# Kernel tuning notes

Measured on AMD Instinct MI355X. Metric: run time of the kernel, lower is better.

## Reference

```python
import jax, jax.numpy as jnp
import numpy as np
from jax import lax

B, L, H, KSIZE = 8, 16384, 128, 65
PAD = KSIZE // 2  # 32; odd kernel keeps output length == L


def setup_inputs() -> dict:
    key = jax.random.key(0)
    kq, kk, kv, kw = jax.random.split(key, 4)
    Q = jax.random.normal(kq, (B, L, H), dtype=jnp.float32)
    K = jax.random.normal(kk, (B, L, H), dtype=jnp.float32)
    V = jax.random.normal(kv, (B, L, H), dtype=jnp.float32)
    # Conv1d weight [out_ch, in_ch, kernel], kaiming-like scale
    W = jax.random.normal(kw, (H, H, KSIZE), dtype=jnp.float32) / np.sqrt(H * KSIZE)
    return {"Q": Q, "K": K, "V": V, "W": W}


def reference(Q, K, V, W):
    # [B, L, H] -> [B, H, L] (channels-first, matching torch transpose(1,2))
    Qt = jnp.swapaxes(Q, 1, 2)
    Kt = jnp.swapaxes(K, 1, 2)
    Vt = jnp.swapaxes(V, 1, 2)
    # Conv1d over sequence dim; lax conv is cross-correlation like torch
    conv_q = lax.conv_general_dilated(
        Qt, W,
        window_strides=(1,),
        padding=[(PAD, PAD)],
        dimension_numbers=("NCH", "OIH", "NCH"),
    )  # [B, H, L]
    scores = conv_q * Kt                      # elementwise gate
    A = jax.nn.softmax(scores, axis=-1)       # softmax over sequence dim
    Z = A * Vt                                # weighted V (elementwise)
    return jnp.swapaxes(Z, 1, 2)              # back to [B, L, H]
```

## Files before the change

kernel.cpp:

```cpp
#include <hip/hip_runtime.h>
#include <stdint.h>

#define BATCH 8
#define LSEQ 16384
#define HDIM 128
#define KSZ 65
#define PADW 32
#define LH (LSEQ*HDIM)
#define TL 256
#define NROWS (TL + 2*PADW)
#define LBLKS (LSEQ/TL)
#define EXP_SHIFT 20.0f
#define SLOT 16384

#define WS_WBF_OFF 4096

typedef __attribute__((ext_vector_type(8))) short bf16x8;
typedef __attribute__((ext_vector_type(4))) short bf16x4;
typedef __attribute__((ext_vector_type(16))) float f32x16;

__device__ __forceinline__ unsigned short f2bf(float f) {
  unsigned int u = __float_as_uint(f);
  return (unsigned short)((u + 0x7FFFu + ((u >> 16) & 1u)) >> 16);
}

__global__ __launch_bounds__(256) void wcvt_kernel(const float* __restrict__ W,
                                                   unsigned short* __restrict__ Wbf) {
  __shared__ float lw[KSZ*HDIM];
  const int o = blockIdx.x;
  const float* src = W + (size_t)o * (HDIM*KSZ);
  for (int t = threadIdx.x; t < HDIM*KSZ; t += 256) lw[t] = src[t];
  __syncthreads();
  const int ob  = o >> 5;
  const int l31 = o & 31;
  for (int idx = threadIdx.x; idx < KSZ*HDIM; idx += 256) {
    const int k = idx >> 7;
    const int i = idx & 127;
    const int kk  = i >> 4;
    const int hi2 = (i >> 3) & 1;
    const int e   = i & 7;
    const size_t dst = (size_t)k*SLOT + kk*2048 + ob*512 + hi2*256 + l31*8 + e;
    Wbf[dst] = f2bf(lw[i*KSZ + k]);
  }
}

__device__ __forceinline__ void stage_tap(const unsigned short* __restrict__ gsrc,
                                          char* lbase, int w, int lane) {
  const char* gb = (const char*)gsrc;
#pragma unroll
  for (int r = 0; r < 4; ++r) {
    const int off = r*8192 + w*1024;
    __builtin_amdgcn_global_load_lds(
        (const __attribute__((address_space(1))) unsigned int*)(gb + off + lane*16),
        (__attribute__((address_space(3))) unsigned int*)(lbase + off),
        16, 0, 0);
  }
}

__global__ __launch_bounds__(512, 2) void conv_gate_kernel(
    const float* __restrict__ Qm, const float* __restrict__ Km,
    const unsigned short* __restrict__ Wfrag,
    float* __restrict__ Eout, float* __restrict__ gsum) {

  __shared__ __align__(16) char smem[147456];
  unsigned short* Qs = (unsigned short*)smem;
  char* WsBase = smem + 81920;

  const int tid  = threadIdx.x;
  const int lane = tid & 63;
  const int w    = tid >> 6;
  const int ks   = w & 1;
  const int wc   = (w >> 1) & 1;
  const int wr   = w >> 2;
  const int l31  = lane & 31;
  const int hi2  = lane >> 5;

  const int bx = blockIdx.x;
  const int b  = bx >> 6;
  const int l0 = (bx & 63) << 8;

  {
    const int r0 = tid >> 5;
    const int c4 = (tid & 31) << 2;
    const float* qbase = Qm + (size_t)b*LH + c4;
#pragma unroll
    for (int it = 0; it < NROWS/16; ++it) {
      const int r = it*16 + r0;
      const int grow = l0 - PADW + r;
      bf16x4 pk = {0, 0, 0, 0};
      if (grow >= 0 && grow < LSEQ) {
        const float4 qv = *(const float4*)(qbase + (size_t)grow*HDIM);
        pk[0] = (short)f2bf(qv.x); pk[1] = (short)f2bf(qv.y);
        pk[2] = (short)f2bf(qv.z); pk[3] = (short)f2bf(qv.w);
      }
      *(bf16x4*)(&Qs[r*HDIM + (c4 ^ ((r & 15) << 3))]) = pk;
    }
  }

  stage_tap(Wfrag, WsBase, w, lane);

  f32x16 acc[4][2] = {};

  __syncthreads();

  const int arow0 = wr*128 + l31;
  const int bbase = (wc*2)*512 + lane*8;

#define LOADC(c, A0,A1,A2,A3,B0,B1) { \
    const int i0 = (ks*64 + (c)*16 + hi2*8) ^ xa; \
    A0 = *(const bf16x8*)(&Qs[(rb     )*HDIM + i0]); \
    A1 = *(const bf16x8*)(&Qs[(rb + 32)*HDIM + i0]); \
    A2 = *(const bf16x8*)(&Qs[(rb + 64)*HDIM + i0]); \
    A3 = *(const bf16x8*)(&Qs[(rb + 96)*HDIM + i0]); \
    B0 = *(const bf16x8*)(&slot[(ks*4 + (c))*2048 + bbase]); \
    B1 = *(const bf16x8*)(&slot[(ks*4 + (c))*2048 + bbase + 512]); \
  }
#define MM(A0,A1,A2,A3,B0,B1) \
    acc[0][0] = __builtin_amdgcn_mfma_f32_32x32x16_bf16(A0, B0, acc[0][0], 0, 0, 0); \
    acc[0][1] = __builtin_amdgcn_mfma_f32_32x32x16_bf16(A0, B1, acc[0][1], 0, 0, 0); \
    acc[1][0] = __builtin_amdgcn_mfma_f32_32x32x16_bf16(A1, B0, acc[1][0], 0, 0, 0); \
    acc[1][1] = __builtin_amdgcn_mfma_f32_32x32x16_bf16(A1, B1, acc[1][1], 0, 0, 0); \
    acc[2][0] = __builtin_amdgcn_mfma_f32_32x32x16_bf16(A2, B0, acc[2][0], 0, 0, 0); \
    acc[2][1] = __builtin_amdgcn_mfma_f32_32x32x16_bf16(A2, B1, acc[2][1], 0, 0, 0); \
    acc[3][0] = __builtin_amdgcn_mfma_f32_32x32x16_bf16(A3, B0, acc[3][0], 0, 0, 0); \
    acc[3][1] = __builtin_amdgcn_mfma_f32_32x32x16_bf16(A3, B1, acc[3][1], 0, 0, 0);

  for (int k = 0; k < KSZ; ++k) {
    const unsigned short* slot = (const unsigned short*)(WsBase + (k & 1)*32768);
    if (k < KSZ-1)
      stage_tap(Wfrag + (size_t)(k+1)*SLOT, WsBase + ((k+1) & 1)*32768, w, lane);

    const int rb = k + arow0;
    const int xa = (rb & 15) << 3;

    bf16x8 a0,a1,a2,a3,b0,b1, c0,c1,c2,c3,d0,d1;
    LOADC(0, a0,a1,a2,a3,b0,b1)
    LOADC(1, c0,c1,c2,c3,d0,d1)
    MM(a0,a1,a2,a3,b0,b1)
    LOADC(2, a0,a1,a2,a3,b0,b1)
    MM(c0,c1,c2,c3,d0,d1)
    LOADC(3, c0,c1,c2,c3,d0,d1)
    MM(a0,a1,a2,a3,b0,b1)
    MM(c0,c1,c2,c3,d0,d1)

    asm volatile("s_waitcnt vmcnt(0)" ::: "memory");
    __builtin_amdgcn_s_barrier();
  }
#undef LOADC
#undef MM

  float* red = (float*)smem;
  const int widx = wr*2 + wc;
  float* reg = red + widx*8192 + lane*4;
  if (ks == 1) {
#pragma unroll
    for (int e4 = 0; e4 < 32; ++e4) {
      const int mfr = e4 >> 3, nf = (e4 >> 2) & 1, r4 = (e4 & 3) << 2;
      float4 v;
      v.x = acc[mfr][nf][r4];   v.y = acc[mfr][nf][r4+1];
      v.z = acc[mfr][nf][r4+2]; v.w = acc[mfr][nf][r4+3];
      *(float4*)(reg + e4*256) = v;
    }
  }
  __syncthreads();

  if (ks == 0) {
#pragma unroll
    for (int e4 = 0; e4 < 32; ++e4) {
      const int mfr = e4 >> 3, nf = (e4 >> 2) & 1, r4 = (e4 & 3) << 2;
      const float4 v = *(const float4*)(reg + e4*256);
      acc[mfr][nf][r4]   += v.x; acc[mfr][nf][r4+1] += v.y;
      acc[mfr][nf][r4+2] += v.z; acc[mfr][nf][r4+3] += v.w;
    }
    float psum[2] = {0.f, 0.f};
#pragma unroll
    for (int mfr = 0; mfr < 4; ++mfr) {
#pragma unroll
      for (int r = 0; r < 16; ++r) {
        const int row = wr*128 + mfr*32 + (r & 3) + 8*(r >> 2) + 4*hi2;
        const size_t gb = (size_t)b*LH + (size_t)(l0 + row)*HDIM + wc*64 + l31;
#pragma unroll
        for (int nf = 0; nf < 2; ++nf) {
          const float s = acc[mfr][nf][r] * Km[gb + nf*32];
          const float e = __expf(s - EXP_SHIFT);
          Eout[gb + nf*32] = e;
          psum[nf] += e;
        }
      }
    }
    psum[0] += __shfl_xor(psum[0], 32);
    psum[1] += __shfl_xor(psum[1], 32);
    if (hi2 == 0) {
      atomicAdd(&gsum[b*HDIM + wc*64 + l31],      psum[0]);
      atomicAdd(&gsum[b*HDIM + wc*64 + 32 + l31], psum[1]);
    }
  }
}

__global__ __launch_bounds__(256) void finalize_kernel(float* __restrict__ out,
                                                       const float* __restrict__ V,
                                                       const float* __restrict__ gsum) {
  const int total4 = (BATCH*LH) >> 2;
  const int stride = gridDim.x * blockDim.x;
  for (int f = blockIdx.x*blockDim.x + threadIdx.x; f < total4; f += stride) {
    const float4 e = ((const float4*)out)[f];
    const float4 v = ((const float4*)V)[f];
    const int e0 = f << 2;
    const float* gs = gsum + ((e0 >> 21) << 7) + (e0 & 127);
    float4 z;
    z.x = e.x * v.x / gs[0];
    z.y = e.y * v.y / gs[1];
    z.z = e.z * v.z / gs[2];
    z.w = e.w * v.w / gs[3];
    ((float4*)out)[f] = z;
  }
}

extern "C" void kernel_launch(void* const* d_in, const int* in_sizes, int n_in,
                              void* d_out, int out_size, void* d_ws, size_t ws_size,
                              hipStream_t stream) {
  (void)in_sizes; (void)n_in; (void)out_size; (void)ws_size;
  const float* Q = (const float*)d_in[0];
  const float* K = (const float*)d_in[1];
  const float* V = (const float*)d_in[2];
  const float* W = (const float*)d_in[3];
  float* out  = (float*)d_out;
  float* gsum = (float*)d_ws;
  unsigned short* Wbf = (unsigned short*)((char*)d_ws + WS_WBF_OFF);

  hipMemsetAsync(d_ws, 0, BATCH*HDIM*sizeof(float), stream);
  wcvt_kernel<<<HDIM, 256, 0, stream>>>(W, Wbf);
  conv_gate_kernel<<<BATCH*LBLKS, 512, 0, stream>>>(Q, K, Wbf, out, gsum);
  finalize_kernel<<<2048, 256, 0, stream>>>(out, V, gsum);
}
```

Baseline: 279.9 us.

## Use 4-wave blocks with 128x128 per-wave-pair tiles for conv MFMA

Cuts the conv kernel block from 8 waves to 4. Each wave now covers all 128 output channels (4x4 MFMA tiles) instead of 64, so every A fragment read from LDS feeds four MFMAs instead of two, which lowers LDS traffic per MFMA. The Q staging and weight-tap staging loops are resized for 256 threads. Accumulators double to 256 fp32 registers per lane, which forces one block per CU (the 144KB LDS already limited residency) and may cause register pressure or spills. The split-K reduction buffer grows to match, and a barrier is added before the LDS region is reused.

```diff
diff --git a/kernel.cpp b/kernel.cpp
--- a/kernel.cpp
+++ b/kernel.cpp
@@ -48,8 +48,8 @@
                                           char* lbase, int w, int lane) {
   const char* gb = (const char*)gsrc;
 #pragma unroll
-  for (int r = 0; r < 4; ++r) {
-    const int off = r*8192 + w*1024;
+  for (int r = 0; r < 8; ++r) {
+    const int off = r*4096 + w*1024;
     __builtin_amdgcn_global_load_lds(
         (const __attribute__((address_space(1))) unsigned int*)(gb + off + lane*16),
         (__attribute__((address_space(3))) unsigned int*)(lbase + off),
@@ -57,7 +57,7 @@
   }
 }
 
-__global__ __launch_bounds__(512, 2) void conv_gate_kernel(
+__global__ __launch_bounds__(256, 1) void conv_gate_kernel(
     const float* __restrict__ Qm, const float* __restrict__ Km,
     const unsigned short* __restrict__ Wfrag,
     float* __restrict__ Eout, float* __restrict__ gsum) {
@@ -70,8 +70,7 @@
   const int lane = tid & 63;
   const int w    = tid >> 6;
   const int ks   = w & 1;
-  const int wc   = (w >> 1) & 1;
-  const int wr   = w >> 2;
+  const int wr   = w >> 1;
   const int l31  = lane & 31;
   const int hi2  = lane >> 5;
 
@@ -84,8 +83,8 @@
     const int c4 = (tid & 31) << 2;
     const float* qbase = Qm + (size_t)b*LH + c4;
 #pragma unroll
-    for (int it = 0; it < NROWS/16; ++it) {
-      const int r = it*16 + r0;
+    for (int it = 0; it < NROWS/8; ++it) {
+      const int r = it*8 + r0;
       const int grow = l0 - PADW + r;
       bf16x4 pk = {0, 0, 0, 0};
       if (grow >= 0 && grow < LSEQ) {
@@ -99,31 +98,12 @@
 
   stage_tap(Wfrag, WsBase, w, lane);
 
-  f32x16 acc[4][2] = {};
+  f32x16 acc[4][4] = {};
 
   __syncthreads();
 
   const int arow0 = wr*128 + l31;
-  const int bbase = (wc*2)*512 + lane*8;
-
-#define LOADC(c, A0,A1,A2,A3,B0,B1) { \
-    const int i0 = (ks*64 + (c)*16 + hi2*8) ^ xa; \
-    A0 = *(const bf16x8*)(&Qs[(rb     )*HDIM + i0]); \
-    A1 = *(const bf16x8*)(&Qs[(rb + 32)*HDIM + i0]); \
-    A2 = *(const bf16x8*)(&Qs[(rb + 64)*HDIM + i0]); \
-    A3 = *(const bf16x8*)(&Qs[(rb + 96)*HDIM + i0]); \
-    B0 = *(const bf16x8*)(&slot[(ks*4 + (c))*2048 + bbase]); \
-    B1 = *(const bf16x8*)(&slot[(ks*4 + (c))*2048 + bbase + 512]); \
-  }
-#define MM(A0,A1,A2,A3,B0,B1) \
-    acc[0][0] = __builtin_amdgcn_mfma_f32_32x32x16_bf16(A0, B0, acc[0][0], 0, 0, 0); \
-    acc[0][1] = __builtin_amdgcn_mfma_f32_32x32x16_bf16(A0, B1, acc[0][1], 0, 0, 0); \
-    acc[1][0] = __builtin_amdgcn_mfma_f32_32x32x16_bf16(A1, B0, acc[1][0], 0, 0, 0); \
-    acc[1][1] = __builtin_amdgcn_mfma_f32_32x32x16_bf16(A1, B1, acc[1][1], 0, 0, 0); \
-    acc[2][0] = __builtin_amdgcn_mfma_f32_32x32x16_bf16(A2, B0, acc[2][0], 0, 0, 0); \
-    acc[2][1] = __builtin_amdgcn_mfma_f32_32x32x16_bf16(A2, B1, acc[2][1], 0, 0, 0); \
-    acc[3][0] = __builtin_amdgcn_mfma_f32_32x32x16_bf16(A3, B0, acc[3][0], 0, 0, 0); \
-    acc[3][1] = __builtin_amdgcn_mfma_f32_32x32x16_bf16(A3, B1, acc[3][1], 0, 0, 0);
+  const int bB = hi2*256 + l31*8;
 
   for (int k = 0; k < KSZ; ++k) {
     const unsigned short* slot = (const unsigned short*)(WsBase + (k & 1)*32768);
@@ -133,66 +113,85 @@
     const int rb = k + arow0;
     const int xa = (rb & 15) << 3;
 
-    bf16x8 a0,a1,a2,a3,b0,b1, c0,c1,c2,c3,d0,d1;
-    LOADC(0, a0,a1,a2,a3,b0,b1)
-    LOADC(1, c0,c1,c2,c3,d0,d1)
-    MM(a0,a1,a2,a3,b0,b1)
-    LOADC(2, a0,a1,a2,a3,b0,b1)
-    MM(c0,c1,c2,c3,d0,d1)
-    LOADC(3, c0,c1,c2,c3,d0,d1)
-    MM(a0,a1,a2,a3,b0,b1)
-    MM(c0,c1,c2,c3,d0,d1)
-
+#pragma unroll
+    for (int c = 0; c < 4; ++c) {
+      const int i0 = (ks*64 + c*16 + hi2*8) ^ xa;
+      bf16x8 A0 = *(const bf16x8*)(&Qs[(rb     )*HDIM + i0]);
+      bf16x8 A1 = *(const bf16x8*)(&Qs[(rb + 32)*HDIM + i0]);
+      bf16x8 A2 = *(const bf16x8*)(&Qs[(rb + 64)*HDIM + i0]);
+      bf16x8 A3 = *(const bf16x8*)(&Qs[(rb + 96)*HDIM + i0]);
+      const unsigned short* bp = slot + (ks*4 + c)*2048 + bB;
+      bf16x8 B0 = *(const bf16x8*)(bp       );
+      bf16x8 B1 = *(const bf16x8*)(bp +  512);
+      bf16x8 B2 = *(const bf16x8*)(bp + 1024);
+      bf16x8 B3 = *(const bf16x8*)(bp + 1536);
+      acc[0][0] = __builtin_amdgcn_mfma_f32_32x32x16_bf16(A0, B0, acc[0][0], 0, 0, 0);
+      acc[0][1] = __builtin_amdgcn_mfma_f32_32x32x16_bf16(A0, B1, acc[0][1], 0, 0, 0);
+      acc[0][2] = __builtin_amdgcn_mfma_f32_32x32x16_bf16(A0, B2, acc[0][2], 0, 0, 0);
+      acc[0][3] = __builtin_amdgcn_mfma_f32_32x32x16_bf16(A0, B3, acc[0][3], 0, 0, 0);
+      acc[1][0] = __builtin_amdgcn_mfma_f32_32x32x16_bf16(A1, B0, acc[1][0], 0, 0, 0);
+      acc[1][1] = __builtin_amdgcn_mfma_f32_32x32x16_bf16(A1, B1, acc[1][1], 0, 0, 0);
+      acc[1][2] = __builtin_amdgcn_mfma_f32_32x32x16_bf16(A1, B2, acc[1][2], 0, 0, 0);
+      acc[1][3] = __builtin_amdgcn_mfma_f32_32x32x16_bf16(A1, B3, acc[1][3], 0, 0, 0);
+      acc[2][0] = __builtin_amdgcn_mfma_f32_32x32x16_bf16(A2, B0, acc[2][0], 0, 0, 0);
+      acc[2][1] = __builtin_amdgcn_mfma_f32_32x32x16_bf16(A2, B1, acc[2][1], 0, 0, 0);
+      acc[2][2] = __builtin_amdgcn_mfma_f32_32x32x16_bf16(A2, B2, acc[2][2], 0, 0, 0);
+      acc[2][3] = __builtin_amdgcn_mfma_f32_32x32x16_bf16(A2, B3, acc[2][3], 0, 0, 0);
+      acc[3][0] = __builtin_amdgcn_mfma_f32_32x32x16_bf16(A3, B0, acc[3][0], 0, 0, 0);
+      acc[3][1] = __builtin_amdgcn_mfma_f32_32x32x16_bf16(A3, B1, acc[3][1], 0, 0, 0);
+      acc[3][2] = __builtin_amdgcn_mfma_f32_32x32x16_bf16(A3, B2, acc[3][2], 0, 0, 0);
+      acc[3][3] = __builtin_amdgcn_mfma_f32_32x32x16_bf16(A3, B3, acc[3][3], 0, 0, 0);
+    }
     asm volatile("s_waitcnt vmcnt(0)" ::: "memory");
     __builtin_amdgcn_s_barrier();
   }
-#undef LOADC
-#undef MM
-
+
+  __syncthreads();
   float* red = (float*)smem;
-  const int widx = wr*2 + wc;
-  float* reg = red + widx*8192 + lane*4;
+  float* reg = red + wr*16384 + lane*4;
   if (ks == 1) {
 #pragma unroll
-    for (int e4 = 0; e4 < 32; ++e4) {
-      const int mfr = e4 >> 3, nf = (e4 >> 2) & 1, r4 = (e4 & 3) << 2;
+    for (int q = 0; q < 64; ++q) {
+      const int mf = q >> 4, nf = (q >> 2) & 3, r4 = (q & 3) << 2;
       float4 v;
-      v.x = acc[mfr][nf][r4];   v.y = acc[mfr][nf][r4+1];
-      v.z = acc[mfr][nf][r4+2]; v.w = acc[mfr][nf][r4+3];
-      *(float4*)(reg + e4*256) = v;
+      v.x = acc[mf][nf][r4];   v.y = acc[mf][nf][r4+1];
+      v.z = acc[mf][nf][r4+2]; v.w = acc[mf][nf][r4+3];
+      *(float4*)(reg + q*256) = v;
     }
   }
   __syncthreads();
 
   if (ks == 0) {
 #pragma unroll
-    for (int e4 = 0; e4 < 32; ++e4) {
-      const int mfr = e4 >> 3, nf = (e4 >> 2) & 1, r4 = (e4 & 3) << 2;
-      const float4 v = *(const float4*)(reg + e4*256);
-      acc[mfr][nf][r4]   += v.x; acc[mfr][nf][r4+1] += v.y;
-      acc[mfr][nf][r4+2] += v.z; acc[mfr][nf][r4+3] += v.w;
-    }
-    float psum[2] = {0.f, 0.f};
-#pragma unroll
-    for (int mfr = 0; mfr < 4; ++mfr) {
+    for (int q = 0; q < 64; ++q) {
+      const int mf = q >> 4, nf = (q >> 2) & 3, r4 = (q & 3) << 2;
+      const float4 v = *(const float4*)(reg + q*256);
+      acc[mf][nf][r4]   += v.x; acc[mf][nf][r4+1] += v.y;
+      acc[mf][nf][r4+2] += v.z; acc[mf][nf][r4+3] += v.w;
+    }
+    float psum[4] = {0.f, 0.f, 0.f, 0.f};
+#pragma unroll
+    for (int mf = 0; mf < 4; ++mf) {
 #pragma unroll
       for (int r = 0; r < 16; ++r) {
-        const int row = wr*128 + mfr*32 + (r & 3) + 8*(r >> 2) + 4*hi2;
-        const size_t gb = (size_t)b*LH + (size_t)(l0 + row)*HDIM + wc*64 + l31;
-#pragma unroll
-        for (int nf = 0; nf < 2; ++nf) {
-          const float s = acc[mfr][nf][r] * Km[gb + nf*32];
+        const int row = wr*128 + mf*32 + (r & 3) + 8*(r >> 2) + 4*hi2;
+        const size_t gb = (size_t)b*LH + (size_t)(l0 + row)*HDIM + l31;
+#pragma unroll
+        for (int nf = 0; nf < 4; ++nf) {
+          const float s = acc[mf][nf][r] * Km[gb + nf*32];
           const float e = __expf(s - EXP_SHIFT);
           Eout[gb + nf*32] = e;
           psum[nf] += e;
         }
       }
     }
-    psum[0] += __shfl_xor(psum[0], 32);
-    psum[1] += __shfl_xor(psum[1], 32);
+#pragma unroll
+    for (int nf = 0; nf < 4; ++nf)
+      psum[nf] += __shfl_xor(psum[nf], 32);
     if (hi2 == 0) {
-      atomicAdd(&gsum[b*HDIM + wc*64 + l31],      psum[0]);
-      atomicAdd(&gsum[b*HDIM + wc*64 + 32 + l31], psum[1]);
+#pragma unroll
+      for (int nf = 0; nf < 4; ++nf)
+        atomicAdd(&gsum[b*HDIM + nf*32 + l31], psum[nf]);
     }
   }
 }
@@ -230,6 +229,6 @@
 
   hipMemsetAsync(d_ws, 0, BATCH*HDIM*sizeof(float), stream);
   wcvt_kernel<<<HDIM, 256, 0, stream>>>(W, Wbf);
-  conv_gate_kernel<<<BATCH*LBLKS, 512, 0, stream>>>(Q, K, Wbf, out, gsum);
+  conv_gate_kernel<<<BATCH*LBLKS, 256, 0, stream>>>(Q, K, Wbf, out, gsum);
   finalize_kernel<<<2048, 256, 0, stream>>>(out, V, gsum);
 }
```

Result: slower. 467.1 us (+66.9%).
